# Kernel optimization log

Measured on AMD Instinct MI355X. Metric: run time of the kernel, lower is better.

## Reference

```python
import jax, jax.numpy as jnp
import numpy as np
import math

B, T, D_MODEL = 1, 2048, 256
N_Q, N_KV = 16, 1
D_HEAD = D_MODEL // N_KV          # 256 (module forces d_head = d_model // n_kv_heads)
QPG = N_Q // N_KV                 # 16
ROPE_BASE = 10000.0
WINDOW = 512
EPS = 1.1920929e-07               # torch finfo(float32).eps (nn.RMSNorm default eps=None)
NEG = -1e30


def _rope(x, base=ROPE_BASE):
    # x: (b, q, g, t, d); interleaved-pair rotary embedding, freq shared per pair
    t, d = x.shape[-2], x.shape[-1]
    freqs = base ** (-2.0 * jnp.arange(d // 2, dtype=jnp.float32) / d)      # (d/2,)
    theta = jnp.arange(t, dtype=jnp.float32)[:, None] * freqs[None, :]     # (t, d/2)
    cos, sin = jnp.cos(theta), jnp.sin(theta)
    x1, x2 = x[..., 0::2], x[..., 1::2]
    r1 = x1 * cos - x2 * sin
    r2 = x1 * sin + x2 * cos
    return jnp.stack([r1, r2], axis=-1).reshape(x.shape)


def _rmsnorm(x, w):
    return x * jax.lax.rsqrt(jnp.mean(x * x, axis=-1, keepdims=True) + EPS) * w


def setup_inputs() -> dict:
    key = jax.random.key(0)
    k0, k1, k2, k3 = jax.random.split(key, 4)
    x = jax.random.normal(k0, (B, T, D_MODEL), dtype=jnp.float32)
    wq = jax.random.normal(k1, (QPG * N_KV * D_HEAD, D_MODEL), dtype=jnp.float32) * 0.02
    wkv = jax.random.normal(k2, (2 * D_HEAD * N_KV, D_MODEL), dtype=jnp.float32) * 0.02
    wo = jax.random.normal(k3, (D_MODEL, D_HEAD * N_Q * N_KV), dtype=jnp.float32) * 0.02
    q_norm_w = jnp.ones((D_HEAD,), dtype=jnp.float32)
    k_norm_w = jnp.ones((D_HEAD,), dtype=jnp.float32)
    return {"x": x, "wq": wq, "wkv": wkv, "wo": wo,
            "q_norm_w": q_norm_w, "k_norm_w": k_norm_w}


def reference(x, wq, wkv, wo, q_norm_w, k_norm_w):
    Bx, Tx, C = x.shape
    q = x @ wq.T                                  # (b, t, qpg*n_kv*d_head)
    kv = x @ wkv.T                                # (b, t, 2*n_kv*d_head)
    k, v = kv[..., :N_KV * D_HEAD], kv[..., N_KV * D_HEAD:]
    # b t q g d -> b q g t d
    q = q.reshape(Bx, Tx, QPG, N_KV, D_HEAD).transpose(0, 2, 3, 1, 4)
    k = k.reshape(Bx, Tx, 1, N_KV, D_HEAD).transpose(0, 2, 3, 1, 4)
    v = v.reshape(Bx, Tx, 1, N_KV, D_HEAD).transpose(0, 2, 3, 1, 4)
    q = _rmsnorm(_rope(q), q_norm_w)
    k = _rmsnorm(_rope(k), k_norm_w)
    rows = jnp.arange(Tx)[:, None]
    cols = jnp.arange(Tx)[None, :]
    mask = (cols <= rows) & ((rows - cols) <= WINDOW)           # causal & sliding window
    scale = 1.0 / math.sqrt(D_HEAD)
    scores = jnp.einsum('bqgtd,bqgsd->bqgts', q, k) * scale     # (b, qpg, n_kv, t, t)
    scores = jnp.where(mask[None, None, None], scores, NEG)
    attn = jax.nn.softmax(scores, axis=-1)
    out = jnp.einsum('bqgts,bqgsd->bqgtd', attn, v)
    out = out.transpose(0, 3, 1, 2, 4).reshape(Bx, Tx, QPG * N_KV * D_HEAD)  # b t (q g d)
    return out @ wo.T
```

## Files before the change

### kernel.cpp

```cpp
#include <hip/hip_runtime.h>

#define TT   2048
#define WIN  512

typedef unsigned short u16;
typedef unsigned long long u64;
typedef __bf16 bf16x8 __attribute__((ext_vector_type(8)));
typedef float  f32x4  __attribute__((ext_vector_type(4)));

__device__ __forceinline__ float bf2f(u16 u){
  unsigned v = ((unsigned)u) << 16;
  return __builtin_bit_cast(float, v);
}
__device__ __forceinline__ u16 f2bf(float f){
  unsigned x = __builtin_bit_cast(unsigned, f);
  unsigned r = x + 0x7fffu + ((x >> 16) & 1u);
  return (u16)(r >> 16);
}
__device__ __forceinline__ f32x4 mfma16(bf16x8 a, bf16x8 b, f32x4 c){
  return __builtin_amdgcn_mfma_f32_16x16x32_bf16(a, b, c, 0, 0, 0);
}
__device__ __forceinline__ bf16x8 ld512(const u16* buf, int row, int byte){
  return *(const bf16x8*)((const char*)buf + row*512 + (byte ^ ((row&7)<<4)));
}
__device__ __forceinline__ bf16x8 ld128(const u16* buf, int row, int byte){
  return *(const bf16x8*)((const char*)buf + row*128 + (byte ^ ((row&7)<<4)));
}
#define GL16(gp, lp) __builtin_amdgcn_global_load_lds( \
    (const __attribute__((address_space(1))) unsigned int*)(gp), \
    (__attribute__((address_space(3))) unsigned int*)(lp), 16, 0, 0)

__global__ __launch_bounds__(64) void k_detect(const u16* __restrict__ x, int* __restrict__ flag){
  int lane = threadIdx.x;
  float mx = 0.f;
  for (int i = lane; i < 2048; i += 64){
    float v = fabsf(bf2f(x[i]));
    mx = (v < 64.0f) ? fmaxf(mx, v) : 1e30f;
  }
  #pragma unroll
  for (int d = 32; d; d >>= 1) mx = fmaxf(mx, __shfl_xor(mx, d));
  if (lane == 0) *flag = (mx < 64.0f) ? 1 : 0;
}

__global__ __launch_bounds__(256) void k_cast(const void* __restrict__ src, u16* __restrict__ dst,
                                              int n4, const int* __restrict__ flag){
  int i = blockIdx.x * 256 + threadIdx.x;
  if (i >= n4) return;
  if (*flag){
    *(u64*)(dst + (size_t)i*4) = *(const u64*)((const u16*)src + (size_t)i*4);
  } else {
    float4 v = *(const float4*)((const float*)src + (size_t)i*4);
    u64 pk = (u64)f2bf(v.x) | ((u64)f2bf(v.y)<<16) | ((u64)f2bf(v.z)<<32) | ((u64)f2bf(v.w)<<48);
    *(u64*)(dst + (size_t)i*4) = pk;
  }
}

__global__ __launch_bounds__(256) void k_wprep(const void* __restrict__ qw, const void* __restrict__ kw,
                                               float* __restrict__ qwf, float* __restrict__ kwf,
                                               const int* __restrict__ flag){
  int i = threadIdx.x;
  int f = *flag;
  qwf[i] = f ? bf2f(((const u16*)qw)[i]) : ((const float*)qw)[i];
  kwf[i] = f ? bf2f(((const u16*)kw)[i]) : ((const float*)kw)[i];
}

__global__ __launch_bounds__(256) void k_tab(float* __restrict__ tab){
  int idx = blockIdx.x * 256 + threadIdx.x;
  int t = idx >> 7, i = idx & 127;
  float fr = exp2f((float)i * (-13.287712379549449f / 128.0f));
  float th = (float)t * fr;
  tab[idx*2 + 0] = cosf(th);
  tab[idx*2 + 1] = sinf(th);
}

__global__ __launch_bounds__(256) void k_qkv(const u16* __restrict__ x, const u16* __restrict__ wq,
                                             const u16* __restrict__ wkv,
                                             u16* __restrict__ q_raw, u16* __restrict__ kv_raw){
  __shared__ __align__(16) u16 Ax[64*256];
  __shared__ __align__(16) u16 Bw[64*256];
  int m0 = blockIdx.x * 64, n0 = blockIdx.y * 64;
  int tid = threadIdx.x;
  const u16* wsrc = (n0 < 4096) ? (wq + (size_t)n0*256) : (wkv + (size_t)(n0-4096)*256);
  int sr = tid >> 5, sk = tid & 31;
  #pragma unroll
  for (int u=0;u<8;++u){
    int r = sr + u*8;
    uint4 a = *(const uint4*)((const char*)(x    + (size_t)(m0+r)*256) + sk*16);
    uint4 b = *(const uint4*)((const char*)(wsrc + (size_t)r*256)      + sk*16);
    *(uint4*)((char*)&Ax[0] + r*512 + ((sk*16) ^ ((r&7)<<4))) = a;
    *(uint4*)((char*)&Bw[0] + r*512 + ((sk*16) ^ ((r&7)<<4))) = b;
  }
  __syncthreads();
  int w = tid>>6, lane = tid&63, ml = lane&15, g = lane>>4;
  int mh = w & 1, nh = w >> 1;
  f32x4 acc[2][2];
  #pragma unroll
  for (int mr=0;mr<2;++mr)
    #pragma unroll
    for (int j=0;j<2;++j) acc[mr][j] = f32x4{0.f,0.f,0.f,0.f};
  #pragma unroll
  for (int kk=0; kk<8; ++kk){
    bf16x8 af[2], bf[2];
    #pragma unroll
    for (int mr=0;mr<2;++mr) af[mr] = ld512(Ax, mh*32 + mr*16 + ml, kk*64 + g*16);
    #pragma unroll
    for (int j=0;j<2;++j)    bf[j]  = ld512(Bw, nh*32 + j*16 + ml,  kk*64 + g*16);
    #pragma unroll
    for (int mr=0;mr<2;++mr)
      #pragma unroll
      for (int j=0;j<2;++j) acc[mr][j] = mfma16(af[mr], bf[j], acc[mr][j]);
  }
  #pragma unroll
  for (int mr=0;mr<2;++mr)
    #pragma unroll
    for (int j=0;j<2;++j)
      #pragma unroll
      for (int r=0;r<4;++r){
        int row = m0 + mh*32 + mr*16 + 4*g + r;
        int n   = n0 + nh*32 + j*16 + ml;
        float v = acc[mr][j][r];
        if (n < 4096) q_raw[(size_t)row*4096 + n] = f2bf(v);
        else          kv_raw[(size_t)row*512 + (n - 4096)] = f2bf(v);
      }
}

__device__ __forceinline__ void rope_norm_row(const u16* __restrict__ src, const float* __restrict__ tab,
                                              const float* __restrict__ wn, u16* __restrict__ dst,
                                              int lane, float post){
  union { u64 q; u16 u[4]; } iv;
  iv.q = *(const u64*)(src + lane*4);
  float v0 = bf2f(iv.u[0]), v1 = bf2f(iv.u[1]), v2 = bf2f(iv.u[2]), v3 = bf2f(iv.u[3]);
  float4 tc = *(const float4*)(tab + lane*4);
  float r0 = v0*tc.x - v1*tc.y;
  float r1 = v0*tc.y + v1*tc.x;
  float r2 = v2*tc.z - v3*tc.w;
  float r3 = v2*tc.w + v3*tc.z;
  float ss = r0*r0 + r1*r1 + r2*r2 + r3*r3;
  #pragma unroll
  for (int d=32; d; d>>=1) ss += __shfl_xor(ss, d);
  float sc = rsqrtf(ss * (1.0f/256.0f) + 1.1920929e-07f) * post;
  u64 pk =  (u64)f2bf(r0*sc*wn[lane*4+0])
         | ((u64)f2bf(r1*sc*wn[lane*4+1]) << 16)
         | ((u64)f2bf(r2*sc*wn[lane*4+2]) << 32)
         | ((u64)f2bf(r3*sc*wn[lane*4+3]) << 48);
  *(u64*)(dst + lane*4) = pk;
}

__global__ __launch_bounds__(256) void k_ropenorm(const u16* __restrict__ q_raw, const u16* __restrict__ kv_raw,
                                                  const float* __restrict__ tab, const float* __restrict__ qw,
                                                  const float* __restrict__ kw, u16* __restrict__ qn,
                                                  u16* __restrict__ kn){
  int row  = blockIdx.x * 4 + (threadIdx.x >> 6);
  int lane = threadIdx.x & 63;
  if (row < 16*2048){
    int h = row >> 11, t = row & 2047;
    rope_norm_row(q_raw + (size_t)t*4096 + h*256, tab + (size_t)t*256, qw,
                  qn + ((size_t)h*2048 + t)*256, lane, 0.0625f);
  } else {
    int t = row - 16*2048;
    rope_norm_row(kv_raw + (size_t)t*512, tab + (size_t)t*256, kw, kn + (size_t)t*256, lane, 1.0f);
  }
}

__global__ __launch_bounds__(256) void k_vtrans(const u16* __restrict__ kv_raw, u16* __restrict__ vt){
  __shared__ u16 Ts[64][72];
  int t0 = blockIdx.x*64, d0 = blockIdx.y*64;
  int tid = threadIdx.x;
  int rr = tid >> 3, c8 = (tid & 7) * 8;
  #pragma unroll
  for (int u=0;u<2;++u){
    int r = rr + u*32;
    uint4 v = *(const uint4*)(kv_raw + (size_t)(t0+r)*512 + 256 + d0 + c8);
    #pragma unroll
    for (int i=0;i<8;++i) Ts[r][c8+i] = ((const u16*)&v)[i];
  }
  __syncthreads();
  #pragma unroll
  for (int u=0;u<2;++u){
    int d = rr + u*32;
    u16 tmp[8];
    #pragma unroll
    for (int i=0;i<8;++i) tmp[i] = Ts[c8+i][d];
    *(uint4*)(vt + (size_t)(d0+d)*2048 + t0 + c8) = *(uint4*)tmp;
  }
}

__global__ __launch_bounds__(512, 2) void k_attn(const u16* __restrict__ qn, const u16* __restrict__ kn,
                                                 const u16* __restrict__ vt, u16* __restrict__ aout){
  __shared__ __align__(16) u16 Ks[2][64*256];
  __shared__ __align__(16) u16 Vs[2][256*64];
  __shared__ __align__(16) u16 Ps[8][16*64];
  int h = blockIdx.x >> 4, qt = blockIdx.x & 15;
  int Q0 = qt * 128;
  int tid = threadIdx.x, w = tid >> 6, lane = tid & 63, ml = lane & 15, g = lane >> 4;
  int s_lo = Q0 - WIN; if (s_lo < 0) s_lo = 0;
  int ntile = (Q0 + 128 - s_lo) >> 6;

  {
    int sr = tid >> 5, sk = tid & 31;
    const u16* qsrc = qn + ((size_t)h*2048 + Q0)*256;
    #pragma unroll
    for (int u=0;u<8;++u){
      int row = sr + u*16;
      uint4 qv = *(const uint4*)((const char*)(qsrc + (size_t)row*256) + sk*16);
      int lr = row & 63;
      *(uint4*)((char*)&Ks[row>>6][0] + lr*512 + ((sk*16) ^ ((lr&7)<<4))) = qv;
    }
  }
  __syncthreads();
  bf16x8 qf[8];
  #pragma unroll
  for (int kk=0; kk<8; ++kk) qf[kk] = ld512(&Ks[w>>2][0], (w&3)*16 + ml, kk*64 + g*16);
  __syncthreads();

  int krow = w*8 + (lane>>5), kslot = lane & 31;
  int vrow = w*32 + (lane>>3), vslot = lane & 7;

  {
    int s0 = s_lo;
    #pragma unroll
    for (int i=0;i<4;++i){
      int r = krow + i*2;
      GL16(kn + (size_t)(s0 + r)*256 + ((kslot ^ (r&7))*8), &Ks[0][(w*8 + i*2)*256]);
    }
    #pragma unroll
    for (int i=0;i<4;++i){
      int d = vrow + i*8;
      GL16(vt + (size_t)d*2048 + s0 + ((vslot ^ (d&7))*8), &Vs[0][(w*32 + i*8)*64]);
    }
  }

  float mx = -1e30f, ls = 0.f;
  f32x4 o[16];
  #pragma unroll
  for (int f=0; f<16; ++f) o[f] = f32x4{0.f,0.f,0.f,0.f};
  int tq = Q0 + w*16 + ml;
  int wmin = Q0 + w*16, wmax = wmin + 15;
  int cur = 0;

  for (int kt=0; kt<ntile; ++kt){
    int s0 = s_lo + kt*64;
    bool haveNext = (kt+1 < ntile);
    if (haveNext){
      int s1 = s0 + 64;
      #pragma unroll
      for (int i=0;i<4;++i){
        int r = krow + i*2;
        GL16(kn + (size_t)(s1 + r)*256 + ((kslot ^ (r&7))*8), &Ks[cur^1][(w*8 + i*2)*256]);
      }
      #pragma unroll
      for (int i=0;i<4;++i){
        int d = vrow + i*8;
        GL16(vt + (size_t)d*2048 + s1 + ((vslot ^ (d&7))*8), &Vs[cur^1][(w*32 + i*8)*64]);
      }
      asm volatile("s_waitcnt vmcnt(8)" ::: "memory");
    } else {
      asm volatile("s_waitcnt vmcnt(0)" ::: "memory");
    }
    __builtin_amdgcn_s_barrier();
    __builtin_amdgcn_sched_barrier(0);

    bool act = (s0 <= wmax) && (s0 + 63 + WIN >= wmin);
    if (act){
      const u16* kb = &Ks[cur][0];
      const u16* vb = &Vs[cur][0];
      f32x4 s[4];
      #pragma unroll
      for (int j=0;j<4;++j) s[j] = f32x4{0.f,0.f,0.f,0.f};
      __builtin_amdgcn_s_setprio(1);
      #pragma unroll
      for (int kk=0; kk<8; ++kk)
        #pragma unroll
        for (int j=0;j<4;++j)
          s[j] = mfma16(ld512(kb, j*16 + ml, kk*64 + g*16), qf[kk], s[j]);
      __builtin_amdgcn_s_setprio(0);
      float best = -1e30f;
      #pragma unroll
      for (int j=0;j<4;++j)
        #pragma unroll
        for (int r=0;r<4;++r){
          int key = s0 + j*16 + 4*g + r;
          float v = s[j][r];
          bool ok = (key <= tq) && (tq - key <= WIN);
          v = ok ? v : -1e30f;
          s[j][r] = v;
          best = fmaxf(best, v);
        }
      best = fmaxf(best, __shfl_xor(best, 16));
      best = fmaxf(best, __shfl_xor(best, 32));
      if (__ballot(best > mx + 8.f)){
        float mn = fmaxf(mx, best);
        float corr = __expf(mx - mn);
        mx = mn; ls *= corr;
        #pragma unroll
        for (int f=0; f<16; ++f) o[f] *= corr;
      }
      float rs = 0.f;
      #pragma unroll
      for (int j=0;j<4;++j){
        u64 pk = 0;
        #pragma unroll
        for (int r=0;r<4;++r){
          float v = s[j][r];
          float p = (v <= -1e29f) ? 0.f : __expf(v - mx);
          rs += p;
          pk |= (u64)f2bf(p) << (16*r);
        }
        *(u64*)((char*)&Ps[w][0] + ml*128 + ((32*j + 8*g) ^ ((ml&7)<<4))) = pk;
      }
      rs += __shfl_xor(rs, 16);
      rs += __shfl_xor(rs, 32);
      ls += rs;
      __builtin_amdgcn_s_setprio(1);
      #pragma unroll
      for (int kk2=0; kk2<2; ++kk2){
        bf16x8 pb = ld128(&Ps[w][0], ml, kk2*64 + g*16);
        #pragma unroll
        for (int f=0; f<16; ++f){
          bf16x8 vf = ld128(vb, f*16 + ml, kk2*64 + g*16);
          o[f] = mfma16(vf, pb, o[f]);
        }
      }
      __builtin_amdgcn_s_setprio(0);
    }
    __builtin_amdgcn_s_barrier();
    __builtin_amdgcn_sched_barrier(0);
    cur ^= 1;
  }
  float inv = 1.0f / ls;
  u16* dst = aout + ((size_t)h*2048 + tq)*256;
  #pragma unroll
  for (int f=0; f<16; ++f){
    f32x4 v = o[f];
    u64 pk = (u64)f2bf(v[0]*inv) | ((u64)f2bf(v[1]*inv)<<16)
           | ((u64)f2bf(v[2]*inv)<<32) | ((u64)f2bf(v[3]*inv)<<48);
    *(u64*)(dst + f*16 + 4*g) = pk;
  }
}

__global__ __launch_bounds__(256) void k_oproj(const u16* __restrict__ aout, const u16* __restrict__ wo,
                                               float* __restrict__ pout){
  __shared__ __align__(16) u16 As[64*256];
  __shared__ __align__(16) u16 Bs[64*256];
  int t0 = blockIdx.x * 64, c0 = blockIdx.y * 64, ksp = blockIdx.z;
  int tid = threadIdx.x, w = tid>>6, lane = tid&63, ml = lane&15, g = lane>>4;
  int mh = w & 1, nh = w >> 1;
  int sr = tid >> 5, sk = tid & 31;
  f32x4 acc[2][2];
  #pragma unroll
  for (int mr=0;mr<2;++mr)
    #pragma unroll
    for (int j=0;j<2;++j) acc[mr][j] = f32x4{0.f,0.f,0.f,0.f};
  for (int kc = ksp*4; kc < ksp*4 + 4; ++kc){
    __syncthreads();
    #pragma unroll
    for (int u=0;u<8;++u){
      int r = sr + u*8;
      uint4 a = *(const uint4*)((const char*)(aout + ((size_t)kc*2048 + t0 + r)*256) + sk*16);
      uint4 b = *(const uint4*)((const char*)(wo + (size_t)(c0+r)*4096 + kc*256) + sk*16);
      *(uint4*)((char*)&As[0] + r*512 + ((sk*16) ^ ((r&7)<<4))) = a;
      *(uint4*)((char*)&Bs[0] + r*512 + ((sk*16) ^ ((r&7)<<4))) = b;
    }
    __syncthreads();
    #pragma unroll
    for (int kk=0; kk<8; ++kk){
      bf16x8 af[2], bf[2];
      #pragma unroll
      for (int mr=0;mr<2;++mr) af[mr] = ld512(As, mh*32 + mr*16 + ml, kk*64 + g*16);
      #pragma unroll
      for (int j=0;j<2;++j)    bf[j]  = ld512(Bs, nh*32 + j*16 + ml,  kk*64 + g*16);
      #pragma unroll
      for (int mr=0;mr<2;++mr)
        #pragma unroll
        for (int j=0;j<2;++j) acc[mr][j] = mfma16(af[mr], bf[j], acc[mr][j]);
    }
  }
  #pragma unroll
  for (int mr=0;mr<2;++mr)
    #pragma unroll
    for (int j=0;j<2;++j)
      #pragma unroll
      for (int r=0;r<4;++r){
        int t = t0 + mh*32 + mr*16 + 4*g + r;
        int c = c0 + nh*32 + j*16 + ml;
        pout[((size_t)ksp*2048 + t)*256 + c] = acc[mr][j][r];
      }
}

__global__ __launch_bounds__(256) void k_red(const float* __restrict__ pout, void* __restrict__ out,
                                             const int* __restrict__ flag){
  int i = blockIdx.x * 256 + threadIdx.x;
  float v = pout[i] + pout[i + 2048*256] + pout[i + 2*2048*256] + pout[i + 3*2048*256];
  if (*flag) ((u16*)out)[i] = f2bf(v);
  else       ((float*)out)[i] = v;
}

extern "C" void kernel_launch(void* const* d_in, const int* in_sizes, int n_in,
                              void* d_out, int out_size, void* d_ws, size_t ws_size,
                              hipStream_t stream) {
  (void)in_sizes; (void)n_in; (void)out_size; (void)ws_size;
  const void* x_r   = d_in[0];
  const void* wq_r  = d_in[1];
  const void* wkv_r = d_in[2];
  const void* wo_r  = d_in[3];
  const void* qw_r  = d_in[4];
  const void* kw_r  = d_in[5];
  char* ws = (char*)d_ws;
  const size_t MB = 1048576;
  u16*   xb     = (u16*)  (ws);
  u16*   wqb    = (u16*)  (ws + 1*MB);
  u16*   wkvb   = (u16*)  (ws + 3*MB);
  u16*   wob    = (u16*)  (ws + 3*MB + MB/2);
  float* tab    = (float*)(ws + 5*MB + MB/2);
  u16*   q_raw  = (u16*)  (ws + 7*MB + MB/2);
  u16*   aout   = q_raw;
  u16*   kv_raw = (u16*)  (ws + 23*MB + MB/2);
  u16*   qn     = (u16*)  (ws + 25*MB + MB/2);
  float* pout   = (float*)qn;
  u16*   kn     = (u16*)  (ws + 41*MB + MB/2);
  u16*   vt     = (u16*)  (ws + 42*MB + MB/2);
  int*   flag   = (int*)  (ws + 43*MB + MB/2);
  float* qwf    = (float*)(ws + 43*MB + MB/2 + 256);
  float* kwf    = (float*)(ws + 43*MB + MB/2 + 1280);

  k_detect<<<dim3(1),   dim3(64),  0, stream>>>((const u16*)x_r, flag);
  k_cast  <<<dim3(512), dim3(256), 0, stream>>>(x_r,   xb,   2048*256/4, flag);
  k_cast  <<<dim3(1024),dim3(256), 0, stream>>>(wq_r,  wqb,  4096*256/4, flag);
  k_cast  <<<dim3(128), dim3(256), 0, stream>>>(wkv_r, wkvb, 512*256/4,  flag);
  k_cast  <<<dim3(1024),dim3(256), 0, stream>>>(wo_r,  wob,  256*4096/4, flag);
  k_wprep <<<dim3(1),   dim3(256), 0, stream>>>(qw_r, kw_r, qwf, kwf, flag);
  k_tab   <<<dim3(1024),dim3(256), 0, stream>>>(tab);
  k_qkv     <<<dim3(32, 72),   dim3(256), 0, stream>>>(xb, wqb, wkvb, q_raw, kv_raw);
  k_ropenorm<<<dim3(8704),     dim3(256), 0, stream>>>(q_raw, kv_raw, tab, qwf, kwf, qn, kn);
  k_vtrans  <<<dim3(32, 4),    dim3(256), 0, stream>>>(kv_raw, vt);
  k_attn    <<<dim3(256),      dim3(512), 0, stream>>>(qn, kn, vt, aout);
  k_oproj   <<<dim3(32, 4, 4), dim3(256), 0, stream>>>(aout, wob, pout);
  k_red     <<<dim3(2048),     dim3(256), 0, stream>>>(pout, d_out, flag);
}
```

Before: 108.8 us.

## Fuse prep kernels, skip casts for bf16 inputs, restructure attention tiling

Merges the rope table, norm-weight prep and four cast kernels into one launch. When inputs are already bf16, the casts are skipped and the GEMMs read the raw buffers directly. The attention kernel changes from 512 threads with 16 query rows per wave and 64-key tiles to 256 threads with 32 query rows per wave and 32-key tiles. Each K/V fragment loaded from LDS now feeds two MFMAs, and Q is loaded straight from global memory into registers. The cost is more accumulator registers per wave, twice as many key-tile iterations and barriers, and a detour through a new LDS swizzle layout.

```diff
diff --git a/kernel.cpp b/kernel.cpp
--- a/kernel.cpp
+++ b/kernel.cpp
@@ -23,8 +23,8 @@
 __device__ __forceinline__ bf16x8 ld512(const u16* buf, int row, int byte){
   return *(const bf16x8*)((const char*)buf + row*512 + (byte ^ ((row&7)<<4)));
 }
-__device__ __forceinline__ bf16x8 ld128(const u16* buf, int row, int byte){
-  return *(const bf16x8*)((const char*)buf + row*128 + (byte ^ ((row&7)<<4)));
+__device__ __forceinline__ bf16x8 ld64s(const u16* buf, int row, int byte){
+  return *(const bf16x8*)((const char*)buf + row*64 + (byte ^ ((row&3)<<4)));
 }
 #define GL16(gp, lp) __builtin_amdgcn_global_load_lds( \
     (const __attribute__((address_space(1))) unsigned int*)(gp), \
@@ -42,42 +42,52 @@
   if (lane == 0) *flag = (mx < 64.0f) ? 1 : 0;
 }
 
-__global__ __launch_bounds__(256) void k_cast(const void* __restrict__ src, u16* __restrict__ dst,
-                                              int n4, const int* __restrict__ flag){
-  int i = blockIdx.x * 256 + threadIdx.x;
-  if (i >= n4) return;
-  if (*flag){
-    *(u64*)(dst + (size_t)i*4) = *(const u64*)((const u16*)src + (size_t)i*4);
-  } else {
-    float4 v = *(const float4*)((const float*)src + (size_t)i*4);
-    u64 pk = (u64)f2bf(v.x) | ((u64)f2bf(v.y)<<16) | ((u64)f2bf(v.z)<<32) | ((u64)f2bf(v.w)<<48);
-    *(u64*)(dst + (size_t)i*4) = pk;
-  }
-}
-
-__global__ __launch_bounds__(256) void k_wprep(const void* __restrict__ qw, const void* __restrict__ kw,
-                                               float* __restrict__ qwf, float* __restrict__ kwf,
-                                               const int* __restrict__ flag){
-  int i = threadIdx.x;
-  int f = *flag;
-  qwf[i] = f ? bf2f(((const u16*)qw)[i]) : ((const float*)qw)[i];
-  kwf[i] = f ? bf2f(((const u16*)kw)[i]) : ((const float*)kw)[i];
-}
-
-__global__ __launch_bounds__(256) void k_tab(float* __restrict__ tab){
-  int idx = blockIdx.x * 256 + threadIdx.x;
-  int t = idx >> 7, i = idx & 127;
-  float fr = exp2f((float)i * (-13.287712379549449f / 128.0f));
-  float th = (float)t * fr;
-  tab[idx*2 + 0] = cosf(th);
-  tab[idx*2 + 1] = sinf(th);
-}
-
-__global__ __launch_bounds__(256) void k_qkv(const u16* __restrict__ x, const u16* __restrict__ wq,
-                                             const u16* __restrict__ wkv,
+__global__ __launch_bounds__(256) void k_prep(const void* __restrict__ x_r, const void* __restrict__ wq_r,
+                                              const void* __restrict__ wkv_r, const void* __restrict__ wo_r,
+                                              const void* __restrict__ qw_r, const void* __restrict__ kw_r,
+                                              u16* __restrict__ xb, u16* __restrict__ wqb,
+                                              u16* __restrict__ wkvb, u16* __restrict__ wob,
+                                              float* __restrict__ tab, float* __restrict__ qwf,
+                                              float* __restrict__ kwf, const int* __restrict__ flag){
+  int b = blockIdx.x, t = threadIdx.x;
+  if (b < 1024){
+    int idx = b*256 + t;
+    int tt = idx >> 7, i = idx & 127;
+    float fr = exp2f((float)i * (-13.287712379549449f / 128.0f));
+    float th = (float)tt * fr;
+    tab[idx*2 + 0] = cosf(th);
+    tab[idx*2 + 1] = sinf(th);
+    return;
+  }
+  if (b == 3712){
+    int f = *flag;
+    qwf[t] = f ? bf2f(((const u16*)qw_r)[t]) : ((const float*)qw_r)[t];
+    kwf[t] = f ? bf2f(((const u16*)kw_r)[t]) : ((const float*)kw_r)[t];
+    return;
+  }
+  if (*flag) return;
+  int cb = b - 1024;
+  const float* s; u16* d; int i;
+  if (cb < 512)       { s=(const float*)x_r;   d=xb;   i = cb*256 + t; }
+  else if (cb < 1536) { s=(const float*)wq_r;  d=wqb;  i = (cb-512)*256 + t; }
+  else if (cb < 1664) { s=(const float*)wkv_r; d=wkvb; i = (cb-1536)*256 + t; }
+  else                { s=(const float*)wo_r;  d=wob;  i = (cb-1664)*256 + t; }
+  float4 v = *(const float4*)(s + (size_t)i*4);
+  u64 pk = (u64)f2bf(v.x) | ((u64)f2bf(v.y)<<16) | ((u64)f2bf(v.z)<<32) | ((u64)f2bf(v.w)<<48);
+  *(u64*)(d + (size_t)i*4) = pk;
+}
+
+__global__ __launch_bounds__(256) void k_qkv(const u16* __restrict__ xb, const u16* __restrict__ wqb,
+                                             const u16* __restrict__ wkvb,
+                                             const void* __restrict__ x_r, const void* __restrict__ wq_r,
+                                             const void* __restrict__ wkv_r, const int* __restrict__ flag,
                                              u16* __restrict__ q_raw, u16* __restrict__ kv_raw){
   __shared__ __align__(16) u16 Ax[64*256];
   __shared__ __align__(16) u16 Bw[64*256];
+  int fl = *flag;
+  const u16* x   = fl ? (const u16*)x_r   : xb;
+  const u16* wq  = fl ? (const u16*)wq_r  : wqb;
+  const u16* wkv = fl ? (const u16*)wkv_r : wkvb;
   int m0 = blockIdx.x * 64, n0 = blockIdx.y * 64;
   int tid = threadIdx.x;
   const u16* wsrc = (n0 < 4096) ? (wq + (size_t)n0*256) : (wkv + (size_t)(n0-4096)*256);
@@ -185,73 +195,64 @@
   }
 }
 
-__global__ __launch_bounds__(512, 2) void k_attn(const u16* __restrict__ qn, const u16* __restrict__ kn,
+__global__ __launch_bounds__(256, 2) void k_attn(const u16* __restrict__ qn, const u16* __restrict__ kn,
                                                  const u16* __restrict__ vt, u16* __restrict__ aout){
-  __shared__ __align__(16) u16 Ks[2][64*256];
-  __shared__ __align__(16) u16 Vs[2][256*64];
-  __shared__ __align__(16) u16 Ps[8][16*64];
+  __shared__ __align__(16) u16 S[36864];
   int h = blockIdx.x >> 4, qt = blockIdx.x & 15;
   int Q0 = qt * 128;
   int tid = threadIdx.x, w = tid >> 6, lane = tid & 63, ml = lane & 15, g = lane >> 4;
+  u16* Pw = S + 32768 + w*1024;
   int s_lo = Q0 - WIN; if (s_lo < 0) s_lo = 0;
-  int ntile = (Q0 + 128 - s_lo) >> 6;
-
-  {
-    int sr = tid >> 5, sk = tid & 31;
-    const u16* qsrc = qn + ((size_t)h*2048 + Q0)*256;
-    #pragma unroll
-    for (int u=0;u<8;++u){
-      int row = sr + u*16;
-      uint4 qv = *(const uint4*)((const char*)(qsrc + (size_t)row*256) + sk*16);
-      int lr = row & 63;
-      *(uint4*)((char*)&Ks[row>>6][0] + lr*512 + ((sk*16) ^ ((lr&7)<<4))) = qv;
-    }
-  }
-  __syncthreads();
-  bf16x8 qf[8];
-  #pragma unroll
-  for (int kk=0; kk<8; ++kk) qf[kk] = ld512(&Ks[w>>2][0], (w&3)*16 + ml, kk*64 + g*16);
-  __syncthreads();
-
-  int krow = w*8 + (lane>>5), kslot = lane & 31;
-  int vrow = w*32 + (lane>>3), vslot = lane & 7;
+  int ntile = (Q0 + 128 - s_lo) >> 5;
+
+  bf16x8 qf[2][8];
+  #pragma unroll
+  for (int mq=0; mq<2; ++mq){
+    const u16* qp = qn + ((size_t)h*2048 + Q0 + w*32 + mq*16 + ml)*256 + 8*g;
+    #pragma unroll
+    for (int kk=0; kk<8; ++kk) qf[mq][kk] = *(const bf16x8*)(qp + kk*32);
+  }
+
+  int krl = lane >> 5, kslot = lane & 31;
+  int vrl = lane >> 2, vslot = lane & 3;
 
   {
     int s0 = s_lo;
     #pragma unroll
     for (int i=0;i<4;++i){
-      int r = krow + i*2;
-      GL16(kn + (size_t)(s0 + r)*256 + ((kslot ^ (r&7))*8), &Ks[0][(w*8 + i*2)*256]);
+      int r = w*8 + i*2 + krl;
+      GL16(kn + (size_t)(s0 + r)*256 + (kslot*8 ^ ((r&7)<<3)), S + (w*8 + i*2)*256);
     }
     #pragma unroll
     for (int i=0;i<4;++i){
-      int d = vrow + i*8;
-      GL16(vt + (size_t)d*2048 + s0 + ((vslot ^ (d&7))*8), &Vs[0][(w*32 + i*8)*64]);
-    }
-  }
-
-  float mx = -1e30f, ls = 0.f;
-  f32x4 o[16];
-  #pragma unroll
-  for (int f=0; f<16; ++f) o[f] = f32x4{0.f,0.f,0.f,0.f};
-  int tq = Q0 + w*16 + ml;
-  int wmin = Q0 + w*16, wmax = wmin + 15;
+      int d = w*64 + i*16 + vrl;
+      GL16(vt + (size_t)d*2048 + s0 + (vslot*8 ^ ((d&3)<<3)), S + 16384 + (w*64 + i*16)*32);
+    }
+  }
+
+  float mx[2] = {-1e30f,-1e30f}, ls[2] = {0.f,0.f};
+  f32x4 o[2][16];
+  #pragma unroll
+  for (int mq=0;mq<2;++mq)
+    #pragma unroll
+    for (int f=0; f<16; ++f) o[mq][f] = f32x4{0.f,0.f,0.f,0.f};
+  int wmin = Q0 + w*32, wmax = wmin + 31;
   int cur = 0;
 
   for (int kt=0; kt<ntile; ++kt){
-    int s0 = s_lo + kt*64;
-    bool haveNext = (kt+1 < ntile);
-    if (haveNext){
-      int s1 = s0 + 64;
+    int s0 = s_lo + kt*32;
+    if (kt+1 < ntile){
+      int s1 = s0 + 32;
+      int nx = cur ^ 1;
       #pragma unroll
       for (int i=0;i<4;++i){
-        int r = krow + i*2;
-        GL16(kn + (size_t)(s1 + r)*256 + ((kslot ^ (r&7))*8), &Ks[cur^1][(w*8 + i*2)*256]);
+        int r = w*8 + i*2 + krl;
+        GL16(kn + (size_t)(s1 + r)*256 + (kslot*8 ^ ((r&7)<<3)), S + nx*8192 + (w*8 + i*2)*256);
       }
       #pragma unroll
       for (int i=0;i<4;++i){
-        int d = vrow + i*8;
-        GL16(vt + (size_t)d*2048 + s1 + ((vslot ^ (d&7))*8), &Vs[cur^1][(w*32 + i*8)*64]);
+        int d = w*64 + i*16 + vrl;
+        GL16(vt + (size_t)d*2048 + s1 + (vslot*8 ^ ((d&3)<<3)), S + 16384 + nx*8192 + (w*64 + i*16)*32);
       }
       asm volatile("s_waitcnt vmcnt(8)" ::: "memory");
     } else {
@@ -260,66 +261,84 @@
     __builtin_amdgcn_s_barrier();
     __builtin_amdgcn_sched_barrier(0);
 
-    bool act = (s0 <= wmax) && (s0 + 63 + WIN >= wmin);
+    bool act = (s0 <= wmax) && (s0 + 31 + WIN >= wmin);
     if (act){
-      const u16* kb = &Ks[cur][0];
-      const u16* vb = &Vs[cur][0];
-      f32x4 s[4];
-      #pragma unroll
-      for (int j=0;j<4;++j) s[j] = f32x4{0.f,0.f,0.f,0.f};
+      const u16* kb = S + cur*8192;
+      const u16* vb = S + 16384 + cur*8192;
+      f32x4 s2[2][2];
+      #pragma unroll
+      for (int mq=0;mq<2;++mq)
+        #pragma unroll
+        for (int j=0;j<2;++j) s2[mq][j] = f32x4{0.f,0.f,0.f,0.f};
       __builtin_amdgcn_s_setprio(1);
       #pragma unroll
       for (int kk=0; kk<8; ++kk)
         #pragma unroll
-        for (int j=0;j<4;++j)
-          s[j] = mfma16(ld512(kb, j*16 + ml, kk*64 + g*16), qf[kk], s[j]);
+        for (int j=0;j<2;++j){
+          bf16x8 kf = ld512(kb, j*16 + ml, kk*64 + g*16);
+          s2[0][j] = mfma16(kf, qf[0][kk], s2[0][j]);
+          s2[1][j] = mfma16(kf, qf[1][kk], s2[1][j]);
+        }
       __builtin_amdgcn_s_setprio(0);
-      float best = -1e30f;
-      #pragma unroll
-      for (int j=0;j<4;++j)
-        #pragma unroll
-        for (int r=0;r<4;++r){
-          int key = s0 + j*16 + 4*g + r;
-          float v = s[j][r];
-          bool ok = (key <= tq) && (tq - key <= WIN);
-          v = ok ? v : -1e30f;
-          s[j][r] = v;
-          best = fmaxf(best, v);
+      float best[2];
+      #pragma unroll
+      for (int mq=0;mq<2;++mq){
+        int tq = Q0 + w*32 + mq*16 + ml;
+        float b = -1e30f;
+        #pragma unroll
+        for (int j=0;j<2;++j)
+          #pragma unroll
+          for (int r=0;r<4;++r){
+            int key = s0 + j*16 + 4*g + r;
+            float v = s2[mq][j][r];
+            bool ok = (key <= tq) && (tq - key <= WIN);
+            v = ok ? v : -1e30f;
+            s2[mq][j][r] = v;
+            b = fmaxf(b, v);
+          }
+        b = fmaxf(b, __shfl_xor(b, 16));
+        b = fmaxf(b, __shfl_xor(b, 32));
+        best[mq] = b;
+      }
+      if (__ballot((best[0] > mx[0] + 8.f) || (best[1] > mx[1] + 8.f))){
+        #pragma unroll
+        for (int mq=0;mq<2;++mq){
+          float mn = fmaxf(mx[mq], best[mq]);
+          float corr = __expf(mx[mq] - mn);
+          mx[mq] = mn; ls[mq] *= corr;
+          #pragma unroll
+          for (int f=0; f<16; ++f) o[mq][f] *= corr;
         }
-      best = fmaxf(best, __shfl_xor(best, 16));
-      best = fmaxf(best, __shfl_xor(best, 32));
-      if (__ballot(best > mx + 8.f)){
-        float mn = fmaxf(mx, best);
-        float corr = __expf(mx - mn);
-        mx = mn; ls *= corr;
-        #pragma unroll
-        for (int f=0; f<16; ++f) o[f] *= corr;
-      }
-      float rs = 0.f;
-      #pragma unroll
-      for (int j=0;j<4;++j){
-        u64 pk = 0;
-        #pragma unroll
-        for (int r=0;r<4;++r){
-          float v = s[j][r];
-          float p = (v <= -1e29f) ? 0.f : __expf(v - mx);
-          rs += p;
-          pk |= (u64)f2bf(p) << (16*r);
+      }
+      #pragma unroll
+      for (int mq=0;mq<2;++mq){
+        int rowp = mq*16 + ml;
+        float rs = 0.f;
+        #pragma unroll
+        for (int j=0;j<2;++j){
+          u64 pk = 0;
+          #pragma unroll
+          for (int r=0;r<4;++r){
+            float v = s2[mq][j][r];
+            float p = (v <= -1e29f) ? 0.f : __expf(v - mx[mq]);
+            rs += p;
+            pk |= (u64)f2bf(p) << (16*r);
+          }
+          *(u64*)((char*)Pw + rowp*64 + ((j*32 + 8*g) ^ ((rowp&3)<<4))) = pk;
         }
-        *(u64*)((char*)&Ps[w][0] + ml*128 + ((32*j + 8*g) ^ ((ml&7)<<4))) = pk;
-      }
-      rs += __shfl_xor(rs, 16);
-      rs += __shfl_xor(rs, 32);
-      ls += rs;
+        rs += __shfl_xor(rs, 16);
+        rs += __shfl_xor(rs, 32);
+        ls[mq] += rs;
+      }
+      bf16x8 pb[2];
+      #pragma unroll
+      for (int mq=0;mq<2;++mq) pb[mq] = ld64s(Pw, mq*16 + ml, g*16);
       __builtin_amdgcn_s_setprio(1);
       #pragma unroll
-      for (int kk2=0; kk2<2; ++kk2){
-        bf16x8 pb = ld128(&Ps[w][0], ml, kk2*64 + g*16);
-        #pragma unroll
-        for (int f=0; f<16; ++f){
-          bf16x8 vf = ld128(vb, f*16 + ml, kk2*64 + g*16);
-          o[f] = mfma16(vf, pb, o[f]);
-        }
+      for (int f=0; f<16; ++f){
+        bf16x8 vf = ld64s(vb, f*16 + ml, g*16);
+        o[0][f] = mfma16(vf, pb[0], o[0][f]);
+        o[1][f] = mfma16(vf, pb[1], o[1][f]);
       }
       __builtin_amdgcn_s_setprio(0);
     }
@@ -327,21 +346,27 @@
     __builtin_amdgcn_sched_barrier(0);
     cur ^= 1;
   }
-  float inv = 1.0f / ls;
-  u16* dst = aout + ((size_t)h*2048 + tq)*256;
-  #pragma unroll
-  for (int f=0; f<16; ++f){
-    f32x4 v = o[f];
-    u64 pk = (u64)f2bf(v[0]*inv) | ((u64)f2bf(v[1]*inv)<<16)
-           | ((u64)f2bf(v[2]*inv)<<32) | ((u64)f2bf(v[3]*inv)<<48);
-    *(u64*)(dst + f*16 + 4*g) = pk;
-  }
-}
-
-__global__ __launch_bounds__(256) void k_oproj(const u16* __restrict__ aout, const u16* __restrict__ wo,
+  #pragma unroll
+  for (int mq=0;mq<2;++mq){
+    float inv = 1.0f / ls[mq];
+    int tq = Q0 + w*32 + mq*16 + ml;
+    u16* dst = aout + ((size_t)h*2048 + tq)*256;
+    #pragma unroll
+    for (int f=0; f<16; ++f){
+      f32x4 v = o[mq][f];
+      u64 pk = (u64)f2bf(v[0]*inv) | ((u64)f2bf(v[1]*inv)<<16)
+             | ((u64)f2bf(v[2]*inv)<<32) | ((u64)f2bf(v[3]*inv)<<48);
+      *(u64*)(dst + f*16 + 4*g) = pk;
+    }
+  }
+}
+
+__global__ __launch_bounds__(256) void k_oproj(const u16* __restrict__ aout, const u16* __restrict__ wob,
+                                               const void* __restrict__ wo_r, const int* __restrict__ flag,
                                                float* __restrict__ pout){
   __shared__ __align__(16) u16 As[64*256];
   __shared__ __align__(16) u16 Bs[64*256];
+  const u16* wo = *flag ? (const u16*)wo_r : wob;
   int t0 = blockIdx.x * 64, c0 = blockIdx.y * 64, ksp = blockIdx.z;
   int tid = threadIdx.x, w = tid>>6, lane = tid&63, ml = lane&15, g = lane>>4;
   int mh = w & 1, nh = w >> 1;
@@ -423,17 +448,14 @@
   float* qwf    = (float*)(ws + 43*MB + MB/2 + 256);
   float* kwf    = (float*)(ws + 43*MB + MB/2 + 1280);
 
-  k_detect<<<dim3(1),   dim3(64),  0, stream>>>((const u16*)x_r, flag);
-  k_cast  <<<dim3(512), dim3(256), 0, stream>>>(x_r,   xb,   2048*256/4, flag);
-  k_cast  <<<dim3(1024),dim3(256), 0, stream>>>(wq_r,  wqb,  4096*256/4, flag);
-  k_cast  <<<dim3(128), dim3(256), 0, stream>>>(wkv_r, wkvb, 512*256/4,  flag);
-  k_cast  <<<dim3(1024),dim3(256), 0, stream>>>(wo_r,  wob,  256*4096/4, flag);
-  k_wprep <<<dim3(1),   dim3(256), 0, stream>>>(qw_r, kw_r, qwf, kwf, flag);
-  k_tab   <<<dim3(1024),dim3(256), 0, stream>>>(tab);
-  k_qkv     <<<dim3(32, 72),   dim3(256), 0, stream>>>(xb, wqb, wkvb, q_raw, kv_raw);
+  k_detect<<<dim3(1),    dim3(64),  0, stream>>>((const u16*)x_r, flag);
+  k_prep  <<<dim3(3713), dim3(256), 0, stream>>>(x_r, wq_r, wkv_r, wo_r, qw_r, kw_r,
+                                                 xb, wqb, wkvb, wob, tab, qwf, kwf, flag);
+  k_qkv     <<<dim3(32, 72),   dim3(256), 0, stream>>>(xb, wqb, wkvb, x_r, wq_r, wkv_r, flag,
+                                                       q_raw, kv_raw);
   k_ropenorm<<<dim3(8704),     dim3(256), 0, stream>>>(q_raw, kv_raw, tab, qwf, kwf, qn, kn);
   k_vtrans  <<<dim3(32, 4),    dim3(256), 0, stream>>>(kv_raw, vt);
-  k_attn    <<<dim3(256),      dim3(512), 0, stream>>>(qn, kn, vt, aout);
-  k_oproj   <<<dim3(32, 4, 4), dim3(256), 0, stream>>>(aout, wob, pout);
+  k_attn    <<<dim3(256),      dim3(256), 0, stream>>>(qn, kn, vt, aout);
+  k_oproj   <<<dim3(32, 4, 4), dim3(256), 0, stream>>>(aout, wob, wo_r, flag, pout);
   k_red     <<<dim3(2048),     dim3(256), 0, stream>>>(pout, d_out, flag);
 }
```

Measured after the change: 147.6 us. 35.7% more time.
